# Kernel optimization log

Measured on AMD Instinct MI355X. Metric: run time of the kernel, lower is better.

The kernel has to match this reference:

```python
import jax, jax.numpy as jnp
import numpy as np
from jax import lax

B, DIM, H, W = 32, 64, 1, 8192
HEADS = 8
EPS_LN = 1e-5
EPS_NORM = 1e-12


def setup_inputs() -> dict:
    key = jax.random.key(0)
    ks = jax.random.split(key, 20)
    g = lambda i, shape, s=0.05: jax.random.normal(ks[i], shape, jnp.float32) * s
    return dict(
        x=jax.random.normal(ks[0], (B, DIM, H, W), jnp.float32),
        qkv_w=g(1, (3 * DIM, DIM)), qkv_b=g(2, (3 * DIM,)),
        dw_w=g(3, (3 * DIM, 1, 3, 3)), dw_b=g(4, (3 * DIM,)),
        proj_w=g(5, (DIM, DIM)), proj_b=g(6, (DIM,)),
        temperature=jnp.ones((HEADS, 1, 1), jnp.float32),
        sp_w=g(7, (DIM,)), sp_b=g(8, (1,)),
        up_w=g(9, (3,)), up_b=g(10, (3,)),
        c2_w=g(11, (1, 1, 2)), c2_b=g(11, (1,)), ln2_w=jnp.ones((W,), jnp.float32), ln2_b=jnp.zeros((W,), jnp.float32),
        c4_w=g(12, (1, 1, 4)), c4_b=g(13, (1,)), ln4_w=jnp.ones((W,), jnp.float32), ln4_b=jnp.zeros((W,), jnp.float32),
        c6_w=g(14, (1, 1, 6)), c6_b=g(15, (1,)), ln6_w=jnp.ones((W,), jnp.float32), ln6_b=jnp.zeros((W,), jnp.float32),
        mp_w=g(16, (DIM,)), mp_b=g(17, (DIM,)),
    )


def _mtl(xs, cw, cb, lw, lb):
    """Multiscale_Temporal_Layer: conv1d 'same' -> LayerNorm(W) -> ELU -> mean pool. xs: (b,1,w)."""
    k = cw.shape[-1]
    tot = k - 1
    lo = tot // 2  # torch 'same': extra pad goes to the right
    y = lax.conv_general_dilated(xs, cw, (1,), [(lo, tot - lo)],
                                 dimension_numbers=('NCH', 'OIH', 'NCH'))
    y = y + cb[None, :, None]
    mu = jnp.mean(y, -1, keepdims=True)
    var = jnp.mean((y - mu) ** 2, -1, keepdims=True)
    y = (y - mu) / jnp.sqrt(var + EPS_LN) * lw + lb
    y = jax.nn.elu(y)
    return jnp.mean(y, -1, keepdims=True)  # (b,1,1)


def _forward(x, qkv_w, qkv_b, dw_w, dw_b, proj_w, proj_b, temperature,
             sp_w, sp_b, up_w, up_b,
             c2_w, c2_b, ln2_w, ln2_b,
             c4_w, c4_b, ln4_w, ln4_b,
             c6_w, c6_b, ln6_w, ln6_b,
             mp_w, mp_b):
    b, c, h, w = x.shape
    hd = c // HEADS  # per-head channel dim
    # 1x1 conv qkv, then depthwise 3x3 conv
    qkv = jnp.einsum('oc,bchw->bohw', qkv_w, x) + qkv_b[None, :, None, None]
    qkv = lax.conv_general_dilated(qkv, dw_w, (1, 1), [(1, 1), (1, 1)],
                                   dimension_numbers=('NCHW', 'OIHW', 'NCHW'),
                                   feature_group_count=3 * c)
    qkv = qkv + dw_b[None, :, None, None]
    q, k, v = jnp.split(qkv, 3, axis=1)
    # Multiscale_Temporal_Attention on v: v is (b,c,1,w)
    xseq = (jnp.einsum('c,bcw->bw', sp_w, v[:, :, 0, :]) + sp_b)[:, None, :]  # (b,1,w)
    up = up_w[None, :, None] * xseq + up_b[None, :, None]  # (b,3,w)
    xx, yy, zz = up[:, 0:1], up[:, 1:2], up[:, 2:3]
    mout = (_mtl(xx, c2_w, c2_b, ln2_w, ln2_b) * xx
            + _mtl(yy, c4_w, c4_b, ln4_w, ln4_b) * yy
            + _mtl(zz, c6_w, c6_b, ln6_w, ln6_b) * zz)  # (b,1,w)
    v = mp_w[None, :, None] * mout + mp_b[None, :, None]  # (b,c,w) via 1x1 conv broadcast
    # channel (transposed) attention over n = h*w tokens
    n = h * w
    q = q.reshape(b, HEADS, hd, n)
    k = k.reshape(b, HEADS, hd, n)
    v = v.reshape(b, HEADS, hd, n)
    q = q / jnp.maximum(jnp.linalg.norm(q, axis=-1, keepdims=True), EPS_NORM)
    k = k / jnp.maximum(jnp.linalg.norm(k, axis=-1, keepdims=True), EPS_NORM)
    attn = jnp.einsum('bhcn,bhdn->bhcd', q, k) * temperature  # (b,heads,hd,hd)
    attn = jax.nn.softmax(attn, axis=-1)
    out = jnp.einsum('bhcd,bhdn->bhcn', attn, v).reshape(b, c, h, w)
    out = jnp.einsum('oc,bchw->bohw', proj_w, out) + proj_b[None, :, None, None]
    return out  # dropouts are identity in eval mode


def reference(x, qkv_w, qkv_b, dw_w, dw_b, proj_w, proj_b, temperature,
              sp_w, sp_b, up_w, up_b,
              c2_w, c2_b, ln2_w, ln2_b,
              c4_w, c4_b, ln4_w, ln4_b,
              c6_w, c6_b, ln6_w, ln6_b,
              mp_w, mp_b):
    return _forward(x, qkv_w, qkv_b, dw_w, dw_b, proj_w, proj_b, temperature,
                    sp_w, sp_b, up_w, up_b,
                    c2_w, c2_b, ln2_w, ln2_b,
                    c4_w, c4_b, ln4_w, ln4_b,
                    c6_w, c6_b, ln6_w, ln6_b,
                    mp_w, mp_b)
```

## Files before the change

### kernel.cpp

```cpp
#include <hip/hip_runtime.h>
#include <hip/hip_bf16.h>
#include <math.h>

#define Wd 8192
#define Bd 32
#define Ttile 64

#define OFF_G    0
#define OFF_H    192
#define OFF_BASE 195
#define OFF_XSEQ 256
#define OFF_PART (256 + Bd*Wd)
#define OFF_S    (OFF_PART + Bd*128*640)
#define OFF_M    (OFF_S + Bd*640)
#define OFF_E    (OFF_M + 96)
#define OFF_F    (OFF_E + Bd*64)
#define OFF_FRAG (OFF_F + Bd*64)

typedef __attribute__((ext_vector_type(8))) short bf16x8;
typedef __attribute__((ext_vector_type(4))) float f32x4;

__device__ __forceinline__ unsigned short f2bf(float v) {
    return __builtin_bit_cast(unsigned short, __float2bfloat16(v));
}
__device__ __forceinline__ float bf2f(unsigned short h) {
    return __builtin_bit_cast(float, (unsigned)h << 16);
}
__device__ __forceinline__ unsigned pk2(float v0, float v1) {
    return (unsigned)f2bf(v0) | ((unsigned)f2bf(v1) << 16);
}

__global__ __launch_bounds__(256) void k0_setup(const float* __restrict__ qkv_w,
                         const float* __restrict__ qkv_b,
                         const float* __restrict__ dw_w, const float* __restrict__ dw_b,
                         const float* __restrict__ sp_w, const float* __restrict__ sp_b,
                         float* __restrict__ ws)
{
    int tid = threadIdx.x;
    if (tid < 192) {
        int j = tid >> 6, ch = tid & 63;
        float acc = 0.f;
        for (int c = 0; c < 64; c++)
            acc += sp_w[c] * dw_w[(128+c)*9 + 3 + j] * qkv_w[(128+c)*64 + ch];
        ws[OFF_G + j*64 + ch] = acc;
    } else if (tid < 195) {
        int j = tid - 192;
        float h = 0.f;
        for (int c = 0; c < 64; c++)
            h += sp_w[c] * dw_w[(128+c)*9 + 3 + j] * qkv_b[128+c];
        ws[OFF_H + j] = h;
    } else if (tid == 195) {
        float base = sp_b[0];
        for (int c = 0; c < 64; c++) base += sp_w[c] * dw_b[128+c];
        ws[OFF_BASE] = base;
    }
    __syncthreads();
    for (int it = tid; it < 36*64; it += 256) {
        int lane = it & 63;
        int cidx = it >> 6;
        int ver = cidx / 18;
        int rem = cidx - ver*18;
        int nt = rem >> 1, kb = rem & 1;
        int row = nt*16 + (lane & 15);
        int ks  = kb*32 + (lane >> 4)*8;
        unsigned short u[8];
        #pragma unroll
        for (int e = 0; e < 8; e++) {
            int k = ks + e;
            float v = 0.f;
            if (row < 128)      v = qkv_w[row*64 + k];
            else if (row < 131) v = ws[OFF_G + (row-128)*64 + k];
            unsigned short h = f2bf(v);
            if (ver == 0) u[e] = h;
            else          u[e] = f2bf(v - bf2f(h));
        }
        unsigned* dst = (unsigned*)(ws + OFF_FRAG) + (ver*1152 + (nt*2+kb)*64 + lane)*4;
        dst[0] = (unsigned)u[0] | ((unsigned)u[1] << 16);
        dst[1] = (unsigned)u[2] | ((unsigned)u[3] << 16);
        dst[2] = (unsigned)u[4] | ((unsigned)u[5] << 16);
        dst[3] = (unsigned)u[6] | ((unsigned)u[7] << 16);
    }
}

#define XT    0
#define QKH   0
#define ZLDS  16384
#define SMEM_BYTES (16384 + 1024)

__global__ __launch_bounds__(256, 5) void k1_main(const float* __restrict__ x,
    const float* __restrict__ qkv_b, const float* __restrict__ dw_w,
    const float* __restrict__ dw_b, float* __restrict__ ws)
{
    __shared__ __align__(16) unsigned char smem[SMEM_BYTES];
    const int tid = threadIdx.x, lane = tid & 63, wv = tid >> 6;
    const int g = lane >> 4, lr = lane & 15;
    const int tile = blockIdx.x, b = blockIdx.y;
    const int w0 = tile * Ttile;
    const float* xb = x + (size_t)b * 64 * Wd;
    const bool safe = (tile != 0) && (tile != 127);

    for (int i = tid; i < 672; i += 256) {
        int j = i >> 5, chp = i & 31;
        int pos0 = w0 - 4 + 4*j;
        float4 a, c;
        if (safe || (unsigned)pos0 < (unsigned)Wd) {
            a = *(const float4*)(xb + (size_t)(2*chp)*Wd + pos0);
            c = *(const float4*)(xb + (size_t)(2*chp+1)*Wd + pos0);
        } else {
            a = (float4){0,0,0,0}; c = (float4){0,0,0,0};
        }
        #pragma unroll
        for (int e = 0; e < 4; e++) {
            int row = 4*j + e;
            unsigned hw = pk2(((const float*)&a)[e], ((const float*)&c)[e]);
            int boff = row*128 + ((((chp>>2) ^ (row & 7)) << 4) | ((chp & 3) << 2));
            *(unsigned*)(smem + XT + boff) = hw;
        }
    }
    __syncthreads();

    f32x4 acc[2][5];
    f32x4 accz[2];
    #pragma unroll
    for (int i = 0; i < 2; i++) {
        accz[i] = (f32x4){0.f,0.f,0.f,0.f};
        #pragma unroll
        for (int m = 0; m < 5; m++) acc[i][m] = (f32x4){0.f,0.f,0.f,0.f};
    }
    const uint4* fragbase = (const uint4*)(ws + OFF_FRAG);

    #pragma unroll
    for (int kb = 0; kb < 2; kb++) {
        bf16x8 axh[5];
        #pragma unroll
        for (int mt = 0; mt < 5; mt++) {
            int row = mt*16 + lr + 3;
            int gran = (kb*4 + g) ^ (row & 7);
            axh[mt] = *(const bf16x8*)(smem + XT + row*128 + gran*16);
        }
        #pragma unroll
        for (int nti = 0; nti < 2; nti++) {
            int nt = wv + nti*4;
            bf16x8 bh = __builtin_bit_cast(bf16x8, fragbase[(nt*2+kb)*64 + lane]);
            bf16x8 bl = __builtin_bit_cast(bf16x8, fragbase[1152 + (nt*2+kb)*64 + lane]);
            #pragma unroll
            for (int mt = 0; mt < 5; mt++) {
                acc[nti][mt] = __builtin_amdgcn_mfma_f32_16x16x32_bf16(axh[mt], bh, acc[nti][mt], 0,0,0);
                acc[nti][mt] = __builtin_amdgcn_mfma_f32_16x16x32_bf16(axh[mt], bl, acc[nti][mt], 0,0,0);
            }
        }
        {
            bf16x8 bzh = __builtin_bit_cast(bf16x8, fragbase[(16+kb)*64 + lane]);
            bf16x8 bzl = __builtin_bit_cast(bf16x8, fragbase[1152 + (16+kb)*64 + lane]);
            int rowz = wv*16 + lr + 3;
            int granz = (kb*4 + g) ^ (rowz & 7);
            bf16x8 azh = *(const bf16x8*)(smem + XT + rowz*128 + granz*16);
            accz[0] = __builtin_amdgcn_mfma_f32_16x16x32_bf16(azh, bzh, accz[0], 0,0,0);
            accz[0] = __builtin_amdgcn_mfma_f32_16x16x32_bf16(azh, bzl, accz[0], 0,0,0);
            if (wv == 0) {
                accz[1] = __builtin_amdgcn_mfma_f32_16x16x32_bf16(axh[4], bzh, accz[1], 0,0,0);
                accz[1] = __builtin_amdgcn_mfma_f32_16x16x32_bf16(axh[4], bzl, accz[1], 0,0,0);
            }
        }
    }
    __syncthreads();

    float* zlds = (float*)(smem + ZLDS);
    #pragma unroll
    for (int nti = 0; nti < 2; nti++) {
        int nt = wv + nti*4;
        int row = nt*16 + lr;
        float bias = qkv_b[row];
        float tb = dw_b[row];
        float t0 = dw_w[row*9+3], t1 = dw_w[row*9+4], t2 = dw_w[row*9+5];
        float4 v[5];
        #pragma unroll
        for (int mt = 0; mt < 5; mt++) {
            #pragma unroll
            for (int r = 0; r < 4; r++) {
                float val = acc[nti][mt][r] + bias;
                if (!safe) {
                    int pos = w0 - 1 + mt*16 + g*4 + r;
                    if (pos < 0 || pos >= Wd) val = 0.f;
                }
                ((float*)&v[mt])[r] = val;
            }
        }
        int src = (lane + 16) & 63;
        #pragma unroll
        for (int mt = 0; mt < 4; mt++) {
            float a0 = __shfl(v[mt].x,   src), b0 = __shfl(v[mt+1].x, src);
            float a1 = __shfl(v[mt].y,   src), b1 = __shfl(v[mt+1].y, src);
            float in4 = (lane < 48) ? a0 : b0;
            float in5 = (lane < 48) ? a1 : b1;
            float o0 = tb + t0*v[mt].x + t1*v[mt].y + t2*v[mt].z;
            float o1 = tb + t0*v[mt].y + t1*v[mt].z + t2*v[mt].w;
            float o2 = tb + t0*v[mt].z + t1*v[mt].w + t2*in4;
            float o3 = tb + t0*v[mt].w + t1*in4     + t2*in5;
            uint2 hw;
            hw.x = pk2(o0, o1);
            hw.y = pk2(o2, o3);
            int gran = (2*mt + (g>>1)) ^ (row & 7);
            int boff = row*128 + (gran << 4) + ((g & 1) << 3);
            *(uint2*)(smem + QKH + boff) = hw;
        }
    }
    if (lr < 3) {
        float4 vz0 = { accz[0][0], accz[0][1], accz[0][2], accz[0][3] };
        *(float4*)(zlds + lr*84 + wv*16 + g*4) = vz0;
        if (wv == 0) {
            float4 vz1 = { accz[1][0], accz[1][1], accz[1][2], accz[1][3] };
            *(float4*)(zlds + lr*84 + 64 + g*4) = vz1;
        }
    }
    __syncthreads();

    if (tid < 64) {
        float a = ws[OFF_BASE];
        #pragma unroll
        for (int j = 0; j < 3; j++) {
            int wg = w0 + tid + j - 1;
            a += zlds[j*84 + tid + j];
            if (wg >= 0 && wg < Wd) a += ws[OFF_H + j];
        }
        ws[OFF_XSEQ + (size_t)b*Wd + w0 + tid] = a;
    }

    {
        const int rq = wv*16 + lr;
        const int rk = 64 + wv*16 + lr;
        f32x4 sqk = (f32x4){0,0,0,0}, sqq = (f32x4){0,0,0,0}, skk = (f32x4){0,0,0,0};
        #pragma unroll
        for (int kb = 0; kb < 2; kb++) {
            int gran = (kb*4 + g) ^ (lr & 7);
            bf16x8 qh = *(const bf16x8*)(smem + QKH + rq*128 + gran*16);
            bf16x8 kh = *(const bf16x8*)(smem + QKH + rk*128 + gran*16);
            sqk = __builtin_amdgcn_mfma_f32_16x16x32_bf16(qh, kh, sqk, 0,0,0);
            sqq = __builtin_amdgcn_mfma_f32_16x16x32_bf16(qh, qh, sqq, 0,0,0);
            skk = __builtin_amdgcn_mfma_f32_16x16x32_bf16(kh, kh, skk, 0,0,0);
        }
        float* pb = ws + OFF_PART + (size_t)(b*128 + tile)*640;
        int hh = lr >> 3, c2 = lr & 7;
        if (hh == (g >> 1)) {
            #pragma unroll
            for (int r = 0; r < 4; r++) {
                int c1 = (g & 1)*4 + r;
                pb[(2*wv + hh)*64 + c1*8 + c2] = sqk[r];
            }
        }
        if ((lr >> 2) == g) {
            int r = lr & 3;
            pb[512 + wv*16 + lr] = sqq[r];
            pb[576 + wv*16 + lr] = skk[r];
        }
    }
}

__device__ __forceinline__ float blk_reduce_256(float v, float* sc) {
    #pragma unroll
    for (int off = 32; off > 0; off >>= 1) v += __shfl_down(v, off, 64);
    __syncthreads();
    if ((threadIdx.x & 63) == 0) sc[threadIdx.x >> 6] = v;
    __syncthreads();
    return sc[0] + sc[1] + sc[2] + sc[3];
}

__global__ __launch_bounds__(256) void k23(const float* __restrict__ ws,
    const float* __restrict__ up_w, const float* __restrict__ up_b,
    const float* __restrict__ c2_w, const float* __restrict__ c2_b,
    const float* __restrict__ ln2_w, const float* __restrict__ ln2_b,
    const float* __restrict__ c4_w, const float* __restrict__ c4_b,
    const float* __restrict__ ln4_w, const float* __restrict__ ln4_b,
    const float* __restrict__ c6_w, const float* __restrict__ c6_b,
    const float* __restrict__ ln6_w, const float* __restrict__ ln6_b,
    float* __restrict__ wsS, float* __restrict__ wsM)
{
    __shared__ float ys[Wd];
    __shared__ float sc[4];
    int bx = blockIdx.x;
    if (bx < 160) {
        int b = bx / 5, chunk = bx - (bx/5)*5;
        int idx = chunk*128 + (threadIdx.x & 127);
        int half = threadIdx.x >> 7;
        const float* part = ws + OFF_PART + (size_t)b*128*640 + idx;
        float s0 = 0.f, s1 = 0.f, s2 = 0.f, s3 = 0.f;
        int t0 = half*64;
        for (int t = t0; t < t0 + 64; t += 4) {
            s0 += part[(size_t)(t  )*640];
            s1 += part[(size_t)(t+1)*640];
            s2 += part[(size_t)(t+2)*640];
            s3 += part[(size_t)(t+3)*640];
        }
        float s = (s0 + s1) + (s2 + s3);
        if (half) ys[threadIdx.x & 127] = s;
        __syncthreads();
        if (!half) wsS[b*640 + idx] = s + ys[threadIdx.x];
        return;
    }
    int t2 = bx - 160;
    int br = t2 >> 5, b = t2 & 31;
    const float *cw, *lw, *lb; float cb; int K, lo;
    if (br == 0)      { cw = c2_w; cb = c2_b[0]; lw = ln2_w; lb = ln2_b; K = 2; lo = 0; }
    else if (br == 1) { cw = c4_w; cb = c4_b[0]; lw = ln4_w; lb = ln4_b; K = 4; lo = 1; }
    else              { cw = c6_w; cb = c6_b[0]; lw = ln6_w; lb = ln6_b; K = 6; lo = 2; }
    float uw = up_w[br], ub = up_b[br];
    const float* xr = ws + OFF_XSEQ + (size_t)b*Wd;

    float s = 0.f, s2 = 0.f;
    for (int w = threadIdx.x; w < Wd; w += 256) {
        float y = cb;
        for (int m = 0; m < K; m++) {
            int p = w + m - lo;
            if (p >= 0 && p < Wd) y += cw[m] * (uw*xr[p] + ub);
        }
        ys[w] = y; s += y; s2 += y*y;
    }
    float mu = blk_reduce_256(s, sc) * (1.f/Wd);
    __syncthreads();
    float Ey2 = blk_reduce_256(s2, sc) * (1.f/Wd);
    float var = fmaxf(Ey2 - mu*mu, 0.f);
    float inv = 1.f / sqrtf(var + 1e-5f);
    float se = 0.f;
    for (int w = threadIdx.x; w < Wd; w += 256) {
        float tt = (ys[w]-mu)*inv*lw[w] + lb[w];
        se += (tt > 0.f) ? tt : expm1f(tt);
    }
    float m = blk_reduce_256(se, sc) * (1.f/Wd);
    if (threadIdx.x == 0) wsM[b*3 + br] = m;
}

__global__ __launch_bounds__(64) void k4_coeffs(const float* __restrict__ ws,
    const float* __restrict__ temperature,
    const float* __restrict__ mp_w, const float* __restrict__ mp_b,
    const float* __restrict__ up_w, const float* __restrict__ up_b,
    const float* __restrict__ proj_w, const float* __restrict__ proj_b,
    float* __restrict__ wsE, float* __restrict__ wsF)
{
    __shared__ float nk[64], alpha[64], beta[64];
    int b = blockIdx.x, t = threadIdx.x;
    const float* Sb = ws + OFF_S + b*640;
    float nq_t = fmaxf(sqrtf(Sb[512 + t]), 1e-12f);
    nk[t]      = fmaxf(sqrtf(Sb[576 + t]), 1e-12f);
    __syncthreads();
    int h = t >> 3;
    float temp = temperature[h];
    float lg[8];
    float mx = -1e30f;
    #pragma unroll
    for (int d = 0; d < 8; d++) {
        lg[d] = Sb[8*t + d] / (nq_t * nk[h*8 + d]) * temp;
        mx = fmaxf(mx, lg[d]);
    }
    float sum = 0.f;
    #pragma unroll
    for (int d = 0; d < 8; d++) { lg[d] = expf(lg[d] - mx); sum += lg[d]; }
    float a = 0.f, bb = 0.f;
    #pragma unroll
    for (int d = 0; d < 8; d++) {
        float at = lg[d] / sum;
        a  += at * mp_w[h*8 + d];
        bb += at * mp_b[h*8 + d];
    }
    alpha[t] = a; beta[t] = bb;
    __syncthreads();
    const float* wm = ws + OFF_M + b*3;
    float m2 = wm[0], m4 = wm[1], m6 = wm[2];
    float A = m2*up_w[0] + m4*up_w[1] + m6*up_w[2];
    float C = m2*up_b[0] + m4*up_b[1] + m6*up_b[2];
    float Pa = 0.f, Pb = 0.f;
    for (int c = 0; c < 64; c++) {
        float pw = proj_w[t*64 + c];
        Pa += pw * alpha[c];
        Pb += pw * beta[c];
    }
    wsE[b*64 + t] = A * Pa;
    wsF[b*64 + t] = C * Pa + Pb + proj_b[t];
}

__global__ __launch_bounds__(256) void k5_out(const float* __restrict__ ws,
                                              float* __restrict__ out)
{
    __shared__ float sE[64], sF[64];
    const int tid = threadIdx.x;
    const int chunk = blockIdx.x, b = blockIdx.y;
    if (tid < 64) {
        sE[tid] = ws[OFF_E + b*64 + tid];
        sF[tid] = ws[OFF_F + b*64 + tid];
    }
    __syncthreads();
    const float4* xs4 = (const float4*)(ws + OFF_XSEQ + (size_t)b*Wd);
    float4 xv = xs4[chunk*128 + (tid & 127)];
    int ohalf = tid >> 7;
    float4* ob = (float4*)out + (size_t)b*64*2048 + chunk*128 + (tid & 127);
    #pragma unroll 8
    for (int oo = 0; oo < 32; oo++) {
        int o = ohalf*32 + oo;
        float e = sE[o], f = sF[o];
        float4 r = { e*xv.x + f, e*xv.y + f, e*xv.z + f, e*xv.w + f };
        ob[(size_t)o*2048] = r;
    }
}

extern "C" void kernel_launch(void* const* d_in, const int* in_sizes, int n_in,
                              void* d_out, int out_size, void* d_ws, size_t ws_size,
                              hipStream_t stream) {
    const float* x      = (const float*)d_in[0];
    const float* qkv_w  = (const float*)d_in[1];
    const float* qkv_b  = (const float*)d_in[2];
    const float* dw_w   = (const float*)d_in[3];
    const float* dw_b   = (const float*)d_in[4];
    const float* proj_w = (const float*)d_in[5];
    const float* proj_b = (const float*)d_in[6];
    const float* temperature = (const float*)d_in[7];
    const float* sp_w   = (const float*)d_in[8];
    const float* sp_b   = (const float*)d_in[9];
    const float* up_w   = (const float*)d_in[10];
    const float* up_b   = (const float*)d_in[11];
    const float* c2_w   = (const float*)d_in[12];
    const float* c2_b   = (const float*)d_in[13];
    const float* ln2_w  = (const float*)d_in[14];
    const float* ln2_b  = (const float*)d_in[15];
    const float* c4_w   = (const float*)d_in[16];
    const float* c4_b   = (const float*)d_in[17];
    const float* ln4_w  = (const float*)d_in[18];
    const float* ln4_b  = (const float*)d_in[19];
    const float* c6_w   = (const float*)d_in[20];
    const float* c6_b   = (const float*)d_in[21];
    const float* ln6_w  = (const float*)d_in[22];
    const float* ln6_b  = (const float*)d_in[23];
    const float* mp_w   = (const float*)d_in[24];
    const float* mp_b   = (const float*)d_in[25];
    float* ws  = (float*)d_ws;
    float* out = (float*)d_out;

    k0_setup<<<1, 256, 0, stream>>>(qkv_w, qkv_b, dw_w, dw_b, sp_w, sp_b, ws);
    k1_main<<<dim3(128, 32), 256, 0, stream>>>(x, qkv_b, dw_w, dw_b, ws);
    k23<<<256, 256, 0, stream>>>(ws, up_w, up_b,
        c2_w, c2_b, ln2_w, ln2_b, c4_w, c4_b, ln4_w, ln4_b, c6_w, c6_b, ln6_w, ln6_b,
        ws + OFF_S, ws + OFF_M);
    k4_coeffs<<<32, 64, 0, stream>>>(ws, temperature, mp_w, mp_b,
        up_w, up_b, proj_w, proj_b, ws + OFF_E, ws + OFF_F);
    k5_out<<<dim3(16, 32), 256, 0, stream>>>(ws, out);
}
```

Measured before the change: 130.5 us.

## Process four tiles per k1 block with register prefetch and fewer partials

```diff
diff --git a/kernel.cpp b/kernel.cpp
--- a/kernel.cpp
+++ b/kernel.cpp
@@ -11,7 +11,7 @@
 #define OFF_BASE 195
 #define OFF_XSEQ 256
 #define OFF_PART (256 + Bd*Wd)
-#define OFF_S    (OFF_PART + Bd*128*640)
+#define OFF_S    (OFF_PART + Bd*32*640)
 #define OFF_M    (OFF_S + Bd*640)
 #define OFF_E    (OFF_M + 96)
 #define OFF_F    (OFF_E + Bd*64)
@@ -36,22 +36,35 @@
                          const float* __restrict__ sp_w, const float* __restrict__ sp_b,
                          float* __restrict__ ws)
 {
+    __shared__ float sw[64*64];
+    __shared__ float sdw[192];
+    __shared__ float ssp[64];
+    __shared__ float sqb[64];
+    __shared__ float sdb[64];
+    __shared__ float sG[192];
     int tid = threadIdx.x;
+    for (int i = tid; i < 4096; i += 256) sw[i] = qkv_w[128*64 + i];
+    if (tid < 192) { int c = tid/3, j = tid - 3*c; sdw[tid] = dw_w[(128+c)*9 + 3 + j]; }
+    if (tid < 64)  { ssp[tid] = sp_w[tid]; sqb[tid] = qkv_b[128+tid]; sdb[tid] = dw_b[128+tid]; }
+    __syncthreads();
     if (tid < 192) {
         int j = tid >> 6, ch = tid & 63;
         float acc = 0.f;
+        #pragma unroll 8
         for (int c = 0; c < 64; c++)
-            acc += sp_w[c] * dw_w[(128+c)*9 + 3 + j] * qkv_w[(128+c)*64 + ch];
-        ws[OFF_G + j*64 + ch] = acc;
+            acc += ssp[c] * sdw[c*3+j] * sw[c*64 + ch];
+        sG[j*64 + ch] = acc;
     } else if (tid < 195) {
         int j = tid - 192;
         float h = 0.f;
+        #pragma unroll 8
         for (int c = 0; c < 64; c++)
-            h += sp_w[c] * dw_w[(128+c)*9 + 3 + j] * qkv_b[128+c];
+            h += ssp[c] * sdw[c*3+j] * sqb[c];
         ws[OFF_H + j] = h;
     } else if (tid == 195) {
         float base = sp_b[0];
-        for (int c = 0; c < 64; c++) base += sp_w[c] * dw_b[128+c];
+        #pragma unroll 8
+        for (int c = 0; c < 64; c++) base += ssp[c] * sdb[c];
         ws[OFF_BASE] = base;
     }
     __syncthreads();
@@ -69,7 +82,7 @@
             int k = ks + e;
             float v = 0.f;
             if (row < 128)      v = qkv_w[row*64 + k];
-            else if (row < 131) v = ws[OFF_G + (row-128)*64 + k];
+            else if (row < 131) v = sG[(row-128)*64 + k];
             unsigned short h = f2bf(v);
             if (ver == 0) u[e] = h;
             else          u[e] = f2bf(v - bf2f(h));
@@ -83,163 +96,203 @@
 }
 
 #define XT    0
-#define QKH   0
-#define ZLDS  16384
-#define SMEM_BYTES (16384 + 1024)
-
-__global__ __launch_bounds__(256, 5) void k1_main(const float* __restrict__ x,
+#define QKH   10752
+#define ZLDS  27136
+#define SMEM_BYTES 28160
+
+__device__ __forceinline__ void load_item(const float* __restrict__ xb, int w0,
+                                          bool safe, int i, uint4& out) {
+    int j = i >> 5, chp = i & 31;
+    int pos0 = w0 - 4 + 4*j;
+    float4 a, c;
+    if (safe || (unsigned)pos0 < (unsigned)Wd) {
+        a = *(const float4*)(xb + (size_t)(2*chp)*Wd + pos0);
+        c = *(const float4*)(xb + (size_t)(2*chp+1)*Wd + pos0);
+    } else {
+        a = (float4){0,0,0,0}; c = (float4){0,0,0,0};
+    }
+    out.x = pk2(a.x, c.x);
+    out.y = pk2(a.y, c.y);
+    out.z = pk2(a.z, c.z);
+    out.w = pk2(a.w, c.w);
+}
+__device__ __forceinline__ void store_item(unsigned char* smem, int i, const uint4& v) {
+    int j = i >> 5, chp = i & 31;
+    const unsigned* pv = &v.x;
+    #pragma unroll
+    for (int e = 0; e < 4; e++) {
+        int row = 4*j + e;
+        int boff = row*128 + ((((chp>>2) ^ (row & 7)) << 4) | ((chp & 3) << 2));
+        *(unsigned*)(smem + XT + boff) = pv[e];
+    }
+}
+
+__global__ __launch_bounds__(256, 4) void k1_main(const float* __restrict__ x,
     const float* __restrict__ qkv_b, const float* __restrict__ dw_w,
     const float* __restrict__ dw_b, float* __restrict__ ws)
 {
     __shared__ __align__(16) unsigned char smem[SMEM_BYTES];
     const int tid = threadIdx.x, lane = tid & 63, wv = tid >> 6;
     const int g = lane >> 4, lr = lane & 15;
-    const int tile = blockIdx.x, b = blockIdx.y;
-    const int w0 = tile * Ttile;
+    const int tg = blockIdx.x, b = blockIdx.y;
     const float* xb = x + (size_t)b * 64 * Wd;
-    const bool safe = (tile != 0) && (tile != 127);
-
-    for (int i = tid; i < 672; i += 256) {
-        int j = i >> 5, chp = i & 31;
-        int pos0 = w0 - 4 + 4*j;
-        float4 a, c;
-        if (safe || (unsigned)pos0 < (unsigned)Wd) {
-            a = *(const float4*)(xb + (size_t)(2*chp)*Wd + pos0);
-            c = *(const float4*)(xb + (size_t)(2*chp+1)*Wd + pos0);
-        } else {
-            a = (float4){0,0,0,0}; c = (float4){0,0,0,0};
-        }
+    const uint4* fragbase = (const uint4*)(ws + OFF_FRAG);
+    float* zlds = (float*)(smem + ZLDS);
+
+    float bias_[2], tb_[2], t0_[2], t1_[2], t2_[2];
+    #pragma unroll
+    for (int nti = 0; nti < 2; nti++) {
+        int row = (wv + nti*4)*16 + lr;
+        bias_[nti] = qkv_b[row];
+        tb_[nti] = dw_b[row];
+        t0_[nti] = dw_w[row*9+3]; t1_[nti] = dw_w[row*9+4]; t2_[nti] = dw_w[row*9+5];
+    }
+
+    f32x4 sqk = (f32x4){0,0,0,0}, sqq = (f32x4){0,0,0,0}, skk = (f32x4){0,0,0,0};
+
+    const bool has3 = (tid < 160);
+    uint4 pf0, pf1, pf2;
+    {
+        bool safe0 = (tg != 0);
+        load_item(xb, tg*256, safe0, tid, pf0);
+        load_item(xb, tg*256, safe0, tid+256, pf1);
+        if (has3) load_item(xb, tg*256, safe0, tid+512, pf2);
+    }
+
+    for (int t = 0; t < 4; ++t) {
+        const int tile = tg*4 + t;
+        const int w0 = tile*Ttile;
+        const bool safe = (tile != 0) && (tile != 127);
+
+        store_item(smem, tid, pf0);
+        store_item(smem, tid+256, pf1);
+        if (has3) store_item(smem, tid+512, pf2);
+        __syncthreads();
+        if (t < 3) {
+            bool safen = ((tile+1) != 127);
+            load_item(xb, w0+64, safen, tid, pf0);
+            load_item(xb, w0+64, safen, tid+256, pf1);
+            if (has3) load_item(xb, w0+64, safen, tid+512, pf2);
+        }
+
+        f32x4 acc[2][5];
+        f32x4 accz0 = (f32x4){0,0,0,0}, accz1 = (f32x4){0,0,0,0};
         #pragma unroll
-        for (int e = 0; e < 4; e++) {
-            int row = 4*j + e;
-            unsigned hw = pk2(((const float*)&a)[e], ((const float*)&c)[e]);
-            int boff = row*128 + ((((chp>>2) ^ (row & 7)) << 4) | ((chp & 3) << 2));
-            *(unsigned*)(smem + XT + boff) = hw;
-        }
-    }
-    __syncthreads();
-
-    f32x4 acc[2][5];
-    f32x4 accz[2];
-    #pragma unroll
-    for (int i = 0; i < 2; i++) {
-        accz[i] = (f32x4){0.f,0.f,0.f,0.f};
+        for (int i = 0; i < 2; i++)
+            #pragma unroll
+            for (int m = 0; m < 5; m++) acc[i][m] = (f32x4){0,0,0,0};
+
         #pragma unroll
-        for (int m = 0; m < 5; m++) acc[i][m] = (f32x4){0.f,0.f,0.f,0.f};
-    }
-    const uint4* fragbase = (const uint4*)(ws + OFF_FRAG);
-
-    #pragma unroll
-    for (int kb = 0; kb < 2; kb++) {
-        bf16x8 axh[5];
-        #pragma unroll
-        for (int mt = 0; mt < 5; mt++) {
-            int row = mt*16 + lr + 3;
-            int gran = (kb*4 + g) ^ (row & 7);
-            axh[mt] = *(const bf16x8*)(smem + XT + row*128 + gran*16);
-        }
+        for (int kb = 0; kb < 2; kb++) {
+            bf16x8 axh[5];
+            #pragma unroll
+            for (int mt = 0; mt < 5; mt++) {
+                int row = mt*16 + lr + 3;
+                int gran = (kb*4 + g) ^ (row & 7);
+                axh[mt] = *(const bf16x8*)(smem + XT + row*128 + gran*16);
+            }
+            #pragma unroll
+            for (int nti = 0; nti < 2; nti++) {
+                int nt = wv + nti*4;
+                bf16x8 bh = __builtin_bit_cast(bf16x8, fragbase[(nt*2+kb)*64 + lane]);
+                bf16x8 bl = __builtin_bit_cast(bf16x8, fragbase[1152 + (nt*2+kb)*64 + lane]);
+                #pragma unroll
+                for (int mt = 0; mt < 5; mt++) {
+                    acc[nti][mt] = __builtin_amdgcn_mfma_f32_16x16x32_bf16(axh[mt], bh, acc[nti][mt], 0,0,0);
+                    acc[nti][mt] = __builtin_amdgcn_mfma_f32_16x16x32_bf16(axh[mt], bl, acc[nti][mt], 0,0,0);
+                }
+            }
+            {
+                bf16x8 bzh = __builtin_bit_cast(bf16x8, fragbase[(16+kb)*64 + lane]);
+                bf16x8 bzl = __builtin_bit_cast(bf16x8, fragbase[1152 + (16+kb)*64 + lane]);
+                int rowz = wv*16 + lr + 3;
+                int granz = (kb*4 + g) ^ (rowz & 7);
+                bf16x8 azh = *(const bf16x8*)(smem + XT + rowz*128 + granz*16);
+                accz0 = __builtin_amdgcn_mfma_f32_16x16x32_bf16(azh, bzh, accz0, 0,0,0);
+                accz0 = __builtin_amdgcn_mfma_f32_16x16x32_bf16(azh, bzl, accz0, 0,0,0);
+                if (wv == 0) {
+                    accz1 = __builtin_amdgcn_mfma_f32_16x16x32_bf16(axh[4], bzh, accz1, 0,0,0);
+                    accz1 = __builtin_amdgcn_mfma_f32_16x16x32_bf16(axh[4], bzl, accz1, 0,0,0);
+                }
+            }
+        }
+
         #pragma unroll
         for (int nti = 0; nti < 2; nti++) {
             int nt = wv + nti*4;
-            bf16x8 bh = __builtin_bit_cast(bf16x8, fragbase[(nt*2+kb)*64 + lane]);
-            bf16x8 bl = __builtin_bit_cast(bf16x8, fragbase[1152 + (nt*2+kb)*64 + lane]);
+            int row = nt*16 + lr;
+            float bias = bias_[nti], tb = tb_[nti];
+            float t0 = t0_[nti], t1 = t1_[nti], t2 = t2_[nti];
+            float4 v[5];
             #pragma unroll
             for (int mt = 0; mt < 5; mt++) {
-                acc[nti][mt] = __builtin_amdgcn_mfma_f32_16x16x32_bf16(axh[mt], bh, acc[nti][mt], 0,0,0);
-                acc[nti][mt] = __builtin_amdgcn_mfma_f32_16x16x32_bf16(axh[mt], bl, acc[nti][mt], 0,0,0);
-            }
-        }
+                #pragma unroll
+                for (int r = 0; r < 4; r++) {
+                    float val = acc[nti][mt][r] + bias;
+                    if (!safe) {
+                        int pos = w0 - 1 + mt*16 + g*4 + r;
+                        if (pos < 0 || pos >= Wd) val = 0.f;
+                    }
+                    ((float*)&v[mt])[r] = val;
+                }
+            }
+            int src = (lane + 16) & 63;
+            #pragma unroll
+            for (int mt = 0; mt < 4; mt++) {
+                float a0 = __shfl(v[mt].x,   src), b0 = __shfl(v[mt+1].x, src);
+                float a1 = __shfl(v[mt].y,   src), b1 = __shfl(v[mt+1].y, src);
+                float in4 = (lane < 48) ? a0 : b0;
+                float in5 = (lane < 48) ? a1 : b1;
+                float o0 = tb + t0*v[mt].x + t1*v[mt].y + t2*v[mt].z;
+                float o1 = tb + t0*v[mt].y + t1*v[mt].z + t2*v[mt].w;
+                float o2 = tb + t0*v[mt].z + t1*v[mt].w + t2*in4;
+                float o3 = tb + t0*v[mt].w + t1*in4     + t2*in5;
+                uint2 hw;
+                hw.x = pk2(o0, o1);
+                hw.y = pk2(o2, o3);
+                int gran = (2*mt + (g>>1)) ^ (row & 7);
+                int boff = row*128 + (gran << 4) + ((g & 1) << 3);
+                *(uint2*)(smem + QKH + boff) = hw;
+            }
+        }
+        if (lr < 3) {
+            float4 vz0 = { accz0[0], accz0[1], accz0[2], accz0[3] };
+            *(float4*)(zlds + lr*84 + wv*16 + g*4) = vz0;
+            if (wv == 0) {
+                float4 vz1 = { accz1[0], accz1[1], accz1[2], accz1[3] };
+                *(float4*)(zlds + lr*84 + 64 + g*4) = vz1;
+            }
+        }
+        __syncthreads();
+
+        if (tid < 64) {
+            float a = ws[OFF_BASE];
+            #pragma unroll
+            for (int j = 0; j < 3; j++) {
+                int wg = w0 + tid + j - 1;
+                a += zlds[j*84 + tid + j];
+                if (wg >= 0 && wg < Wd) a += ws[OFF_H + j];
+            }
+            ws[OFF_XSEQ + (size_t)b*Wd + w0 + tid] = a;
+        }
+
         {
-            bf16x8 bzh = __builtin_bit_cast(bf16x8, fragbase[(16+kb)*64 + lane]);
-            bf16x8 bzl = __builtin_bit_cast(bf16x8, fragbase[1152 + (16+kb)*64 + lane]);
-            int rowz = wv*16 + lr + 3;
-            int granz = (kb*4 + g) ^ (rowz & 7);
-            bf16x8 azh = *(const bf16x8*)(smem + XT + rowz*128 + granz*16);
-            accz[0] = __builtin_amdgcn_mfma_f32_16x16x32_bf16(azh, bzh, accz[0], 0,0,0);
-            accz[0] = __builtin_amdgcn_mfma_f32_16x16x32_bf16(azh, bzl, accz[0], 0,0,0);
-            if (wv == 0) {
-                accz[1] = __builtin_amdgcn_mfma_f32_16x16x32_bf16(axh[4], bzh, accz[1], 0,0,0);
-                accz[1] = __builtin_amdgcn_mfma_f32_16x16x32_bf16(axh[4], bzl, accz[1], 0,0,0);
-            }
-        }
-    }
-    __syncthreads();
-
-    float* zlds = (float*)(smem + ZLDS);
-    #pragma unroll
-    for (int nti = 0; nti < 2; nti++) {
-        int nt = wv + nti*4;
-        int row = nt*16 + lr;
-        float bias = qkv_b[row];
-        float tb = dw_b[row];
-        float t0 = dw_w[row*9+3], t1 = dw_w[row*9+4], t2 = dw_w[row*9+5];
-        float4 v[5];
-        #pragma unroll
-        for (int mt = 0; mt < 5; mt++) {
-            #pragma unroll
-            for (int r = 0; r < 4; r++) {
-                float val = acc[nti][mt][r] + bias;
-                if (!safe) {
-                    int pos = w0 - 1 + mt*16 + g*4 + r;
-                    if (pos < 0 || pos >= Wd) val = 0.f;
-                }
-                ((float*)&v[mt])[r] = val;
-            }
-        }
-        int src = (lane + 16) & 63;
-        #pragma unroll
-        for (int mt = 0; mt < 4; mt++) {
-            float a0 = __shfl(v[mt].x,   src), b0 = __shfl(v[mt+1].x, src);
-            float a1 = __shfl(v[mt].y,   src), b1 = __shfl(v[mt+1].y, src);
-            float in4 = (lane < 48) ? a0 : b0;
-            float in5 = (lane < 48) ? a1 : b1;
-            float o0 = tb + t0*v[mt].x + t1*v[mt].y + t2*v[mt].z;
-            float o1 = tb + t0*v[mt].y + t1*v[mt].z + t2*v[mt].w;
-            float o2 = tb + t0*v[mt].z + t1*v[mt].w + t2*in4;
-            float o3 = tb + t0*v[mt].w + t1*in4     + t2*in5;
-            uint2 hw;
-            hw.x = pk2(o0, o1);
-            hw.y = pk2(o2, o3);
-            int gran = (2*mt + (g>>1)) ^ (row & 7);
-            int boff = row*128 + (gran << 4) + ((g & 1) << 3);
-            *(uint2*)(smem + QKH + boff) = hw;
-        }
-    }
-    if (lr < 3) {
-        float4 vz0 = { accz[0][0], accz[0][1], accz[0][2], accz[0][3] };
-        *(float4*)(zlds + lr*84 + wv*16 + g*4) = vz0;
-        if (wv == 0) {
-            float4 vz1 = { accz[1][0], accz[1][1], accz[1][2], accz[1][3] };
-            *(float4*)(zlds + lr*84 + 64 + g*4) = vz1;
-        }
-    }
-    __syncthreads();
-
-    if (tid < 64) {
-        float a = ws[OFF_BASE];
-        #pragma unroll
-        for (int j = 0; j < 3; j++) {
-            int wg = w0 + tid + j - 1;
-            a += zlds[j*84 + tid + j];
-            if (wg >= 0 && wg < Wd) a += ws[OFF_H + j];
-        }
-        ws[OFF_XSEQ + (size_t)b*Wd + w0 + tid] = a;
+            const int rq = wv*16 + lr;
+            const int rk = 64 + wv*16 + lr;
+            #pragma unroll
+            for (int kb = 0; kb < 2; kb++) {
+                int gran = (kb*4 + g) ^ (lr & 7);
+                bf16x8 qh = *(const bf16x8*)(smem + QKH + rq*128 + gran*16);
+                bf16x8 kh = *(const bf16x8*)(smem + QKH + rk*128 + gran*16);
+                sqk = __builtin_amdgcn_mfma_f32_16x16x32_bf16(qh, kh, sqk, 0,0,0);
+                sqq = __builtin_amdgcn_mfma_f32_16x16x32_bf16(qh, qh, sqq, 0,0,0);
+                skk = __builtin_amdgcn_mfma_f32_16x16x32_bf16(kh, kh, skk, 0,0,0);
+            }
+        }
     }
 
     {
-        const int rq = wv*16 + lr;
-        const int rk = 64 + wv*16 + lr;
-        f32x4 sqk = (f32x4){0,0,0,0}, sqq = (f32x4){0,0,0,0}, skk = (f32x4){0,0,0,0};
-        #pragma unroll
-        for (int kb = 0; kb < 2; kb++) {
-            int gran = (kb*4 + g) ^ (lr & 7);
-            bf16x8 qh = *(const bf16x8*)(smem + QKH + rq*128 + gran*16);
-            bf16x8 kh = *(const bf16x8*)(smem + QKH + rk*128 + gran*16);
-            sqk = __builtin_amdgcn_mfma_f32_16x16x32_bf16(qh, kh, sqk, 0,0,0);
-            sqq = __builtin_amdgcn_mfma_f32_16x16x32_bf16(qh, qh, sqq, 0,0,0);
-            skk = __builtin_amdgcn_mfma_f32_16x16x32_bf16(kh, kh, skk, 0,0,0);
-        }
-        float* pb = ws + OFF_PART + (size_t)(b*128 + tile)*640;
+        float* pb = ws + OFF_PART + (size_t)(b*32 + tg)*640;
         int hh = lr >> 3, c2 = lr & 7;
         if (hh == (g >> 1)) {
             #pragma unroll
@@ -282,10 +335,10 @@
         int b = bx / 5, chunk = bx - (bx/5)*5;
         int idx = chunk*128 + (threadIdx.x & 127);
         int half = threadIdx.x >> 7;
-        const float* part = ws + OFF_PART + (size_t)b*128*640 + idx;
+        const float* part = ws + OFF_PART + (size_t)b*32*640 + idx;
         float s0 = 0.f, s1 = 0.f, s2 = 0.f, s3 = 0.f;
-        int t0 = half*64;
-        for (int t = t0; t < t0 + 64; t += 4) {
+        int t0 = half*16;
+        for (int t = t0; t < t0 + 16; t += 4) {
             s0 += part[(size_t)(t  )*640];
             s1 += part[(size_t)(t+1)*640];
             s2 += part[(size_t)(t+2)*640];
@@ -434,7 +487,7 @@
     float* out = (float*)d_out;
 
     k0_setup<<<1, 256, 0, stream>>>(qkv_w, qkv_b, dw_w, dw_b, sp_w, sp_b, ws);
-    k1_main<<<dim3(128, 32), 256, 0, stream>>>(x, qkv_b, dw_w, dw_b, ws);
+    k1_main<<<dim3(32, 32), 256, 0, stream>>>(x, qkv_b, dw_w, dw_b, ws);
     k23<<<256, 256, 0, stream>>>(ws, up_w, up_b,
         c2_w, c2_b, ln2_w, ln2_b, c4_w, c4_b, ln4_w, ln4_b, c6_w, c6_b, ln6_w, ln6_b,
         ws + OFF_S, ws + OFF_M);
```

Result: slower. 206.3 us (+58.1%).
